# Kernel optimization log

Measured on AMD Instinct MI355X. Metric: run time of the kernel, lower is better.

## Reference

```python
import jax, jax.numpy as jnp
import numpy as np

N = 50000
NUM_GRAPHS = 64
EPS = 1e-16  # PyG softmax denominator epsilon


def _gat_conv(x, src, dst, W, a_src, a_dst, b, heads, out_ch):
    n = x.shape[0]
    h = (x @ W).reshape(n, heads, out_ch)                    # [N,H,C]
    al_s = jnp.einsum('nhc,hc->nh', h, a_src)                # [N,H]
    al_d = jnp.einsum('nhc,hc->nh', h, a_dst)                # [N,H]
    e = jax.nn.leaky_relu(al_s[src] + al_d[dst], 0.2)        # [E,H]
    emax = jax.ops.segment_max(e, dst, num_segments=n)       # [N,H]
    ee = jnp.exp(e - emax[dst])
    den = jax.ops.segment_sum(ee, dst, num_segments=n)       # [N,H]
    alpha = ee / (den[dst] + EPS)                            # [E,H]
    msg = h[src] * alpha[:, :, None]                         # [E,H,C]
    out = jax.ops.segment_sum(msg, dst, num_segments=n)      # [N,H,C]
    return out.reshape(n, heads * out_ch) + b


def setup_inputs() -> dict:
    key = jax.random.key(0)
    ks = jax.random.split(key, 16)
    E = 250000
    x = jax.random.normal(ks[0], (N, 11), dtype=jnp.float32)
    edge_index = jax.random.randint(ks[1], (2, E), 0, N, dtype=jnp.int64)
    batch = jnp.sort(jax.random.randint(ks[2], (N,), 0, NUM_GRAPHS, dtype=jnp.int64))
    def glorot(k, shape):
        fan = shape[0] + shape[-1]
        return jax.random.uniform(k, shape, jnp.float32, -1.0, 1.0) * np.sqrt(6.0 / fan)
    return {
        'x': x, 'edge_index': edge_index, 'batch': batch,
        'W1': glorot(ks[3], (11, 8 * 128)),
        'a1s': glorot(ks[4], (8, 128)), 'a1d': glorot(ks[5], (8, 128)),
        'b1': jnp.zeros((8 * 128,), jnp.float32),
        'W2': glorot(ks[6], (1024, 8 * 64)),
        'a2s': glorot(ks[7], (8, 64)), 'a2d': glorot(ks[8], (8, 64)),
        'b2': jnp.zeros((8 * 64,), jnp.float32),
        'W3': glorot(ks[9], (512, 4 * 32)),
        'a3s': glorot(ks[10], (4, 32)), 'a3d': glorot(ks[11], (4, 32)),
        'b3': jnp.zeros((4 * 32,), jnp.float32),
        'Wout': glorot(ks[12], (128, 1)),
        'bout': jnp.zeros((1,), jnp.float32),
    }


def reference(x, edge_index, batch, W1, a1s, a1d, b1, W2, a2s, a2d, b2,
              W3, a3s, a3d, b3, Wout, bout):
    n = x.shape[0]
    # GATConv adds self-loops by default
    loop = jnp.arange(n, dtype=edge_index.dtype)
    src = jnp.concatenate([edge_index[0], loop])
    dst = jnp.concatenate([edge_index[1], loop])
    h = jax.nn.leaky_relu(_gat_conv(x, src, dst, W1, a1s, a1d, b1, 8, 128), 0.01)
    h = jax.nn.leaky_relu(_gat_conv(h, src, dst, W2, a2s, a2d, b2, 8, 64), 0.01)
    h = jax.nn.leaky_relu(_gat_conv(h, src, dst, W3, a3s, a3d, b3, 4, 32), 0.01)
    # global mean pool over graphs
    sums = jax.ops.segment_sum(h, batch, num_segments=NUM_GRAPHS)      # [G,128]
    cnt = jax.ops.segment_sum(jnp.ones((n,), h.dtype), batch, num_segments=NUM_GRAPHS)
    pooled = sums / jnp.maximum(cnt, 1.0)[:, None]
    return pooled @ Wout + bout                                        # [G,1]
```

## Files before the change

### kernel.cpp

```cpp
#include <hip/hip_runtime.h>

#define EPS 1e-16f

typedef __attribute__((ext_vector_type(8))) short short8;
typedef __attribute__((ext_vector_type(4))) float f32x4;

__device__ __forceinline__ float b2f(unsigned short u) {
    return __uint_as_float(((unsigned)u) << 16);
}
__device__ __forceinline__ unsigned short f2b(float f) {
    unsigned u = __float_as_uint(f);
    u += 0x7fffu + ((u >> 16) & 1u);
    return (unsigned short)(u >> 16);
}

typedef __attribute__((address_space(3))) void lds_vp;
typedef __attribute__((address_space(1))) const void glb_vp;
__device__ __forceinline__ void load_lds16(const unsigned short* g,
                                           unsigned short* l) {
    __builtin_amdgcn_global_load_lds((glb_vp*)g, (lds_vp*)l, 16, 0, 0);
}

__global__ void setup_kernel(const float* __restrict__ W1,
                             const float* __restrict__ W2,
                             const float* __restrict__ W3,
                             unsigned short* __restrict__ wt2,
                             unsigned short* __restrict__ wt3,
                             unsigned short* __restrict__ w1sk,
                             const float* __restrict__ a1s,
                             const float* __restrict__ a1d,
                             float* __restrict__ w_as,
                             float* __restrict__ w_ad, int* __restrict__ deg,
                             float* __restrict__ pool, int N, int GC, int WB,
                             int DB, int PB) {
    int b = blockIdx.x, t = threadIdx.x;
    if (b < WB) {
        int i = b * 256 + t;
        if (i < 1024 * 512) {
            int k = i / 512, n = i % 512;
            wt2[(size_t)n * 1024 + k] = f2b(W2[i]);
        } else if (i < 1024 * 512 + 512 * 128) {
            int j = i - 1024 * 512;
            int k = j / 128, n = j % 128;
            wt3[(size_t)n * 512 + k] = f2b(W3[j]);
        } else if (i < 1024 * 512 + 512 * 128 + 8 * 128 * 32) {
            int q = i - (1024 * 512 + 512 * 128);
            int h = q >> 12, rem = q & 4095;
            int c = rem >> 5, kk = rem & 31;
            int off = (h == 7) ? 16 : 0;
            float v = 0.f;
            int k = kk - off;
            if (k >= 0 && k < 11) v = W1[k * 1024 + h * 128 + c];
            w1sk[q] = f2b(v);
        }
    } else if (b < WB + DB) {
        int i = (b - WB) * 256 + t;
        if (i < N) deg[i] = 1;
    } else if (b < WB + DB + PB) {
        int i = (b - WB - DB) * 256 + t;
        if (i < GC) pool[i] = 0.f;
    } else {
        if (t < 88) {
            int h = t / 11, k = t % 11;
            float s = 0.f, d = 0.f;
            for (int c = 0; c < 128; c++) {
                float w = W1[k * 1024 + h * 128 + c];
                s += w * a1s[h * 128 + c];
                d += w * a1d[h * 128 + c];
            }
            w_as[h * 16 + k] = s;
            w_ad[h * 16 + k] = d;
        }
    }
}

__global__ void hist_al1_kernel(const int* __restrict__ ei, int E, int N,
                                int* __restrict__ deg,
                                const float* __restrict__ x,
                                const float* __restrict__ w_as,
                                const float* __restrict__ w_ad,
                                float* __restrict__ als,
                                float* __restrict__ ald, int EB) {
    int b = blockIdx.x, t = threadIdx.x;
    if (b < EB) {
        int e = b * 256 + t;
        if (e < E) {
            int d = ei[E + e];
            if ((unsigned)d < (unsigned)N) atomicAdd(&deg[d], 1);
        }
    } else {
        int i = (b - EB) * 256 + t;
        if (i < N * 8) {
            int n = i >> 3, h = i & 7;
            float s = 0.f, d = 0.f;
#pragma unroll
            for (int k = 0; k < 11; k++) {
                float xv = x[n * 11 + k];
                s += xv * w_as[h * 16 + k];
                d += xv * w_ad[h * 16 + k];
            }
            als[i] = s;
            ald[i] = d;
        }
    }
}

__global__ void scan_block_kernel(const int* __restrict__ deg,
                                  int* __restrict__ rowst,
                                  int* __restrict__ bsum, int N) {
    __shared__ int s[256];
    int t = threadIdx.x, b = blockIdx.x;
    int i = b * 256 + t;
    s[t] = (i < N) ? deg[i] : 0;
    __syncthreads();
    for (int o = 1; o < 256; o <<= 1) {
        int a = (t >= o) ? s[t - o] : 0;
        __syncthreads();
        s[t] += a;
        __syncthreads();
    }
    if (i < N) rowst[i + 1] = s[t];
    if (t == 255) bsum[b] = s[255];
}

__global__ void scan_top_kernel(const int* __restrict__ bsum,
                                int* __restrict__ boff, int NB) {
    __shared__ int psum[65];
    int t = threadIdx.x;
    int chunk = (NB + 63) / 64;
    int lo = t * chunk, hi = lo + chunk;
    if (lo > NB) lo = NB;
    if (hi > NB) hi = NB;
    int s = 0;
    for (int i = lo; i < hi; i++) s += bsum[i];
    psum[t + 1] = s;
    __syncthreads();
    if (t == 0) {
        psum[0] = 0;
        for (int i = 1; i <= 64; i++) psum[i] += psum[i - 1];
    }
    __syncthreads();
    int run = psum[t];
    for (int i = lo; i < hi; i++) {
        boff[i] = run;
        run += bsum[i];
    }
}

__global__ void scan_finish_kernel(int* __restrict__ rowst,
                                   const int* __restrict__ boff,
                                   const int* __restrict__ deg,
                                   int* __restrict__ srcs,
                                   int* __restrict__ cursor, int N) {
    int i = blockIdx.x * 256 + threadIdx.x;
    if (i == 0) rowst[0] = 0;
    if (i < N) {
        int incl = rowst[i + 1] + boff[blockIdx.x];
        rowst[i + 1] = incl;
        int st = incl - deg[i];
        srcs[st] = i;
        cursor[i] = st + 1;
    }
}

__global__ void scatter_kernel(const int* __restrict__ ei, int E, int N,
                               int* cursor, int* srcs) {
    int e = blockIdx.x * blockDim.x + threadIdx.x;
    if (e < E) {
        int d = ei[E + e];
        if ((unsigned)d < (unsigned)N) {
            int p = atomicAdd(&cursor[d], 1);
            int s = ei[e];
            if ((unsigned)s >= (unsigned)N) s = d;
            srcs[p] = s;
        }
    }
}

__global__ void agg1_fused(const float* __restrict__ x,
                           const float* __restrict__ als,
                           const float* __restrict__ ald,
                           const int* __restrict__ rowst,
                           const int* __restrict__ srcs,
                           unsigned short* __restrict__ A2, int N) {
    constexpr int MAXE = 64;
    __shared__ float sv[MAXE * 8];
    __shared__ float sx[MAXE * 12];
    int n = blockIdx.x;
    int t = threadIdx.x;
    int h = t >> 4, k = t & 15;
    int start = rowst[n], end = rowst[n + 1];
    int deg = end - start;
    float acc = 0.f;

    if (deg <= MAXE) {
        for (int p = t; p < deg * 8; p += 128) {
            int e = p >> 3, hh = p & 7;
            int s = srcs[start + e];
            float v = als[s * 8 + hh] + ald[n * 8 + hh];
            sv[e * 8 + hh] = v > 0.f ? v : 0.2f * v;
        }
        for (int p = t; p < deg * 16; p += 128) {
            int e = p >> 4, kx = p & 15;
            if (kx < 11)
                sx[e * 12 + kx] = x[(size_t)srcs[start + e] * 11 + kx];
        }
        __syncthreads();
        float m = -1e30f;
        for (int e = k; e < deg; e += 16) m = fmaxf(m, sv[e * 8 + h]);
#pragma unroll
        for (int o = 1; o < 16; o <<= 1) m = fmaxf(m, __shfl_xor(m, o));
        float ee[(MAXE + 15) / 16];
        float den = 0.f;
        {
            int kk = 0;
            for (int e = k; e < deg; e += 16, kk++) {
                float xv = expf(sv[e * 8 + h] - m);
                ee[kk] = xv;
                den += xv;
            }
        }
#pragma unroll
        for (int o = 1; o < 16; o <<= 1) den += __shfl_xor(den, o);
        float dinv = 1.0f / (den + EPS);
        {
            int kk = 0;
            for (int e = k; e < deg; e += 16, kk++)
                sv[e * 8 + h] = ee[kk] * dinv;
        }
        __syncthreads();
        const int CH = 4;
        for (int e = 0; e < deg; e += CH) {
            int mc = deg - e;
            if (mc > CH) mc = CH;
            float al[CH], xv[CH];
#pragma unroll
            for (int j = 0; j < CH; j++)
                if (j < mc) {
                    al[j] = sv[(e + j) * 8 + h];
                    xv[j] = (k < 11) ? sx[(e + j) * 12 + k] : 0.f;
                }
#pragma unroll
            for (int j = 0; j < CH; j++)
                if (j < mc) acc += al[j] * xv[j];
        }
    } else {
        float aldn = ald[n * 8 + h];
        float m = -1e30f;
        for (int idx = start + k; idx < end; idx += 16) {
            float v = als[srcs[idx] * 8 + h] + aldn;
            v = v > 0.f ? v : 0.2f * v;
            m = fmaxf(m, v);
        }
#pragma unroll
        for (int o = 1; o < 16; o <<= 1) m = fmaxf(m, __shfl_xor(m, o));
        float den = 0.f;
        for (int idx = start + k; idx < end; idx += 16) {
            float v = als[srcs[idx] * 8 + h] + aldn;
            v = v > 0.f ? v : 0.2f * v;
            den += expf(v - m);
        }
#pragma unroll
        for (int o = 1; o < 16; o <<= 1) den += __shfl_xor(den, o);
        float dinv = 1.0f / (den + EPS);
        for (int idx = start; idx < end; idx++) {
            int s = srcs[idx];
            float v = als[s * 8 + h] + aldn;
            v = v > 0.f ? v : 0.2f * v;
            float a = expf(v - m) * dinv;
            float xv = (k < 11) ? x[s * 11 + k] : 0.f;
            acc += a * xv;
        }
    }
    A2[(size_t)n * 128 + t] = f2b(acc);
}

template <bool EPI, int HB, int CC, bool SK>
__global__ __launch_bounds__(256) void gemm_mfma(
    const unsigned short* __restrict__ A, const unsigned short* __restrict__ Bt,
    unsigned short* __restrict__ C, const float* __restrict__ bias,
    const float* __restrict__ a_s, const float* __restrict__ a_d,
    float* __restrict__ als, float* __restrict__ ald, int H, int M, int N,
    int K, int lda) {
    int NX = gridDim.x;
    int bid = blockIdx.y * NX + blockIdx.x;
    int win = bid & (8 * NX - 1);
    int mg = bid / (8 * NX);
    int m_t = mg * 8 + (win & 7);
    int n_t = win >> 3;
    int bm = m_t * 128, bn = n_t * 128;
    if (bm >= M) return;

    union SMem {
        struct {
            unsigned short As[2][128 * 32];
            unsigned short Bs[2][128 * 32];
        } k;
        unsigned short Ct[128 * 132];
    };
    __shared__ __align__(16) SMem sm;
    auto& As = sm.k.As;
    auto& Bs = sm.k.Bs;
    auto& Ct = sm.Ct;

    int t = threadIdx.x;
    int w = t >> 6, lane = t & 63;
    int quad = lane >> 4, l16 = lane & 15;
    int wr = (w >> 1) * 64, wc = (w & 1) * 64;

    int kofs = 0;
    const unsigned short* Bb = Bt;
    if (SK) {
        kofs = n_t * 16;
        if (kofs > lda - 32) kofs = lda - 32;
        Bb = Bt + (size_t)n_t * 128 * 32;
    }

    int c0 = w * 128 + lane;
    int c1 = c0 + 64;
    int r0 = c0 >> 2, p0 = c0 & 3;
    int r1 = c1 >> 2, p1 = c1 & 3;
    int j0 = (p0 - (r0 >> 1)) & 3;
    int j1 = (p1 - (r1 >> 1)) & 3;
    int ga0 = bm + r0;
    if (ga0 >= M) ga0 = M - 1;
    int ga1 = bm + r1;
    if (ga1 >= M) ga1 = M - 1;
    const unsigned short* Ag0 = A + (size_t)ga0 * lda + kofs + j0 * 8;
    const unsigned short* Ag1 = A + (size_t)ga1 * lda + kofs + j1 * 8;
    size_t br0 = SK ? (size_t)r0 : (size_t)(bn + r0);
    size_t br1 = SK ? (size_t)r1 : (size_t)(bn + r1);
    const unsigned short* Bg0 = Bb + br0 * K + j0 * 8;
    const unsigned short* Bg1 = Bb + br1 * K + j1 * 8;

    auto stage = [&](int st, int k0) {
        load_lds16(Ag0 + k0, &As[st][(w * 128) * 8]);
        load_lds16(Ag1 + k0, &As[st][(w * 128 + 64) * 8]);
        load_lds16(Bg0 + k0, &Bs[st][(w * 128) * 8]);
        load_lds16(Bg1 + k0, &Bs[st][(w * 128 + 64) * 8]);
    };

    int aoff[4], boff4[4];
#pragma unroll
    for (int i = 0; i < 4; i++) {
        int ra = wr + i * 16 + l16;
        aoff[i] = ra * 32 + (((quad + (ra >> 1)) & 3) * 8);
        int rb = wc + i * 16 + l16;
        boff4[i] = rb * 32 + (((quad + (rb >> 1)) & 3) * 8);
    }

    f32x4 acc[4][4] = {};
    stage(0, 0);
    int st = 0;
    for (int k0 = 0; k0 < K; k0 += 32, st ^= 1) {
        __syncthreads();
        if (k0 + 32 < K) stage(st ^ 1, k0 + 32);
        short8 a[4], b[4];
#pragma unroll
        for (int mi = 0; mi < 4; mi++) a[mi] = *(const short8*)&As[st][aoff[mi]];
#pragma unroll
        for (int ni = 0; ni < 4; ni++) b[ni] = *(const short8*)&Bs[st][boff4[ni]];
#pragma unroll
        for (int mi = 0; mi < 4; mi++)
#pragma unroll
            for (int ni = 0; ni < 4; ni++)
                acc[mi][ni] = __builtin_amdgcn_mfma_f32_16x16x32_bf16(
                    a[mi], b[ni], acc[mi][ni], 0, 0, 0);
    }
    __syncthreads();

#pragma unroll
    for (int mi = 0; mi < 4; mi++) {
#pragma unroll
        for (int r = 0; r < 4; r++) {
            int rl = wr + mi * 16 + quad * 4 + r;
#pragma unroll
            for (int ni = 0; ni < 4; ni++) {
                int cl = wc + ni * 16 + l16;
                float v = acc[mi][ni][r];
                if (EPI) {
                    v += bias[bn + cl];
                    v = v > 0.f ? v : 0.01f * v;
                }
                Ct[rl * 132 + cl] = f2b(v);
            }
        }
    }
    __syncthreads();
#pragma unroll
    for (int p = 0; p < 16; p++) {
        int q = p * 256 + t;
        int row = q >> 5, c8 = q & 31;
        if (bm + row < M) {
            uint2 v = *(const uint2*)&Ct[row * 132 + c8 * 4];
            *(uint2*)&C[(size_t)(bm + row) * N + bn + c8 * 4] = v;
        }
    }
    if (HB > 0) {
        for (int pi = t; pi < 128 * HB; pi += 256) {
            int row = pi / HB, hl = pi % HB;
            if (bm + row >= M) continue;
            int hg = bn / CC + hl;
            const unsigned short* rp = &Ct[row * 132 + hl * CC];
            const float* asp = a_s + hg * CC;
            const float* adp = a_d + hg * CC;
            float s = 0.f, d = 0.f;
#pragma unroll
            for (int c = 0; c < CC; c++) {
                float v = b2f(rp[c]);
                s += v * asp[c];
                d += v * adp[c];
            }
            als[(size_t)(bm + row) * H + hg] = s;
            ald[(size_t)(bm + row) * H + hg] = d;
        }
    }
}

template <int HB, int CC>
__global__ __launch_bounds__(256, 2) void gemm_pipe(
    const unsigned short* __restrict__ A, const unsigned short* __restrict__ Bt,
    unsigned short* __restrict__ C, const float* __restrict__ a_s,
    const float* __restrict__ a_d, float* __restrict__ als,
    float* __restrict__ ald, int H, int M, int N, int K) {
    int NX = gridDim.x;
    int bid = blockIdx.y * NX + blockIdx.x;
    int win = bid & (8 * NX - 1);
    int mg = bid / (8 * NX);
    int m_t = mg * 8 + (win & 7);
    int n_t = win >> 3;
    int bm = m_t * 128, bn = n_t * 128;
    if (bm >= M) return;

    union SMem {
        struct {
            unsigned short As[2][128 * 64];
            unsigned short Bs[2][128 * 64];
        } k;
        unsigned short Ct[128 * 132];
    };
    __shared__ __align__(16) SMem sm;

    int t = threadIdx.x;
    int w = t >> 6, lane = t & 63;
    int quad = lane >> 4, l16 = lane & 15;
    int wr = (w >> 1) * 64, wc = (w & 1) * 64;

    int srow = lane >> 3;
    int gsl = (lane & 7) ^ srow;
    const unsigned short* Ag[4];
    const unsigned short* Bg[4];
#pragma unroll
    for (int j = 0; j < 4; j++) {
        int row = (j * 4 + w) * 8 + srow;
        int ga = bm + row;
        if (ga > M - 1) ga = M - 1;
        Ag[j] = A + (size_t)ga * K + gsl * 8;
        Bg[j] = Bt + (size_t)(bn + row) * K + gsl * 8;
    }
    auto stage = [&](int st, int kt) {
        int ko = kt * 64;
#pragma unroll
        for (int j = 0; j < 4; j++) {
            load_lds16(Ag[j] + ko, &sm.k.As[st][(j * 4 + w) * 512]);
            load_lds16(Bg[j] + ko, &sm.k.Bs[st][(j * 4 + w) * 512]);
        }
    };

    int arow[4], brow[4];
#pragma unroll
    for (int i = 0; i < 4; i++) {
        arow[i] = (wr + i * 16 + l16) * 64;
        brow[i] = (wc + i * 16 + l16) * 64;
    }
    int sw = l16 & 7;

    f32x4 acc[4][4] = {};
    int NT = K >> 6;
    stage(0, 0);
    if (NT > 1) stage(1, 1);
    for (int tt = 0; tt < NT; tt++) {
        int bb = tt & 1;
        if (tt + 1 < NT)
            asm volatile("s_waitcnt vmcnt(8)" ::: "memory");
        else
            asm volatile("s_waitcnt vmcnt(0)" ::: "memory");
        __builtin_amdgcn_s_barrier();
        __builtin_amdgcn_sched_barrier(0);
#pragma unroll
        for (int ks = 0; ks < 2; ks++) {
            short8 a[4], b[4];
            int so = ((ks * 4 + quad) ^ sw) * 8;
#pragma unroll
            for (int mi = 0; mi < 4; mi++)
                a[mi] = *(const short8*)&sm.k.As[bb][arow[mi] + so];
#pragma unroll
            for (int ni = 0; ni < 4; ni++)
                b[ni] = *(const short8*)&sm.k.Bs[bb][brow[ni] + so];
            __builtin_amdgcn_s_setprio(1);
#pragma unroll
            for (int mi = 0; mi < 4; mi++)
#pragma unroll
                for (int ni = 0; ni < 4; ni++)
                    acc[mi][ni] = __builtin_amdgcn_mfma_f32_16x16x32_bf16(
                        a[mi], b[ni], acc[mi][ni], 0, 0, 0);
            __builtin_amdgcn_s_setprio(0);
        }
        asm volatile("s_waitcnt lgkmcnt(0)" ::: "memory");
        __builtin_amdgcn_s_barrier();
        if (tt + 2 < NT) stage(bb, tt + 2);
    }
    __syncthreads();

#pragma unroll
    for (int mi = 0; mi < 4; mi++) {
#pragma unroll
        for (int r = 0; r < 4; r++) {
            int rl = wr + mi * 16 + quad * 4 + r;
#pragma unroll
            for (int ni = 0; ni < 4; ni++) {
                int cl = wc + ni * 16 + l16;
                sm.Ct[rl * 132 + cl] = f2b(acc[mi][ni][r]);
            }
        }
    }
    __syncthreads();
#pragma unroll
    for (int p = 0; p < 16; p++) {
        int q = p * 256 + t;
        int row = q >> 5, c8 = q & 31;
        if (bm + row < M) {
            uint2 v = *(const uint2*)&sm.Ct[row * 132 + c8 * 4];
            *(uint2*)&C[(size_t)(bm + row) * N + bn + c8 * 4] = v;
        }
    }
    if (HB > 0) {
        for (int pi = t; pi < 128 * HB; pi += 256) {
            int row = pi / HB, hl = pi % HB;
            if (bm + row >= M) continue;
            int hg = bn / CC + hl;
            const unsigned short* rp = &sm.Ct[row * 132 + hl * CC];
            const float* asp = a_s + hg * CC;
            const float* adp = a_d + hg * CC;
            float s = 0.f, d = 0.f;
#pragma unroll
            for (int c = 0; c < CC; c++) {
                float v = b2f(rp[c]);
                s += v * asp[c];
                d += v * adp[c];
            }
            als[(size_t)(bm + row) * H + hg] = s;
            ald[(size_t)(bm + row) * H + hg] = d;
        }
    }
}

template <int H, int C>
__global__ void agg_fused4(const unsigned short* __restrict__ hin,
                           const float* __restrict__ als,
                           const float* __restrict__ ald,
                           const int* __restrict__ rowst,
                           const int* __restrict__ srcs,
                           const float* __restrict__ bias,
                           unsigned short* __restrict__ out, int N) {
    constexpr int HC = H * C;
    constexpr int NT = HC / 4;
    constexpr int TPH = C / 4;
    constexpr int MAXE = 64;
    __shared__ float sv[MAXE * H];
    __shared__ int ssrc[MAXE];
    int n = blockIdx.x;
    int t = threadIdx.x;
    int c = t * 4;
    int hh = c / C;
    int li = (c % C) / 4;
    int start = rowst[n], end = rowst[n + 1];
    int deg = end - start;
    float a0 = 0.f, a1 = 0.f, a2 = 0.f, a3 = 0.f;

    if (deg <= MAXE) {
        for (int p = t; p < deg * H; p += NT) {
            int e = p / H, h = p % H;
            int s = srcs[start + e];
            if (h == 0) ssrc[e] = s;
            float v = als[s * H + h] + ald[n * H + h];
            sv[e * H + h] = v > 0.f ? v : 0.2f * v;
        }
        __syncthreads();
        float m = -1e30f;
        for (int e = li; e < deg; e += TPH) m = fmaxf(m, sv[e * H + hh]);
#pragma unroll
        for (int o = 1; o < TPH; o <<= 1) m = fmaxf(m, __shfl_xor(m, o));
        float ee[(MAXE + TPH - 1) / TPH];
        float den = 0.f;
        {
            int k = 0;
            for (int e = li; e < deg; e += TPH, k++) {
                float x = expf(sv[e * H + hh] - m);
                ee[k] = x;
                den += x;
            }
        }
#pragma unroll
        for (int o = 1; o < TPH; o <<= 1) den += __shfl_xor(den, o);
        float dinv = 1.0f / (den + EPS);
        {
            int k = 0;
            for (int e = li; e < deg; e += TPH, k++)
                sv[e * H + hh] = ee[k] * dinv;
        }
        __syncthreads();
        const int CH = 4;
        for (int e = 0; e < deg; e += CH) {
            int mc = deg - e;
            if (mc > CH) mc = CH;
            int ss[CH];
            float al[CH];
            ushort4 uv[CH];
#pragma unroll
            for (int j = 0; j < CH; j++)
                if (j < mc) {
                    ss[j] = ssrc[e + j];
                    al[j] = sv[(e + j) * H + hh];
                }
#pragma unroll
            for (int j = 0; j < CH; j++)
                if (j < mc)
                    uv[j] = *(const ushort4*)(hin + (size_t)ss[j] * HC + c);
#pragma unroll
            for (int j = 0; j < CH; j++)
                if (j < mc) {
                    a0 += al[j] * b2f(uv[j].x);
                    a1 += al[j] * b2f(uv[j].y);
                    a2 += al[j] * b2f(uv[j].z);
                    a3 += al[j] * b2f(uv[j].w);
                }
        }
    } else {
        float aldn = ald[n * H + hh];
        float m = -1e30f;
        for (int idx = start + li; idx < end; idx += TPH) {
            float v = als[srcs[idx] * H + hh] + aldn;
            v = v > 0.f ? v : 0.2f * v;
            m = fmaxf(m, v);
        }
#pragma unroll
        for (int o = 1; o < TPH; o <<= 1) m = fmaxf(m, __shfl_xor(m, o));
        float den = 0.f;
        for (int idx = start + li; idx < end; idx += TPH) {
            float v = als[srcs[idx] * H + hh] + aldn;
            v = v > 0.f ? v : 0.2f * v;
            den += expf(v - m);
        }
#pragma unroll
        for (int o = 1; o < TPH; o <<= 1) den += __shfl_xor(den, o);
        float dinv = 1.0f / (den + EPS);
        const int CH = 4;
        for (int idx = start; idx < end; idx += CH) {
            int mc = end - idx;
            if (mc > CH) mc = CH;
            int ss[CH];
            float lv[CH];
            ushort4 uv[CH];
#pragma unroll
            for (int j = 0; j < CH; j++)
                if (j < mc) ss[j] = srcs[idx + j];
#pragma unroll
            for (int j = 0; j < CH; j++)
                if (j < mc) lv[j] = als[ss[j] * H + hh];
#pragma unroll
            for (int j = 0; j < CH; j++)
                if (j < mc)
                    uv[j] = *(const ushort4*)(hin + (size_t)ss[j] * HC + c);
#pragma unroll
            for (int j = 0; j < CH; j++)
                if (j < mc) {
                    float v = lv[j] + aldn;
                    v = v > 0.f ? v : 0.2f * v;
                    float a = expf(v - m) * dinv;
                    a0 += a * b2f(uv[j].x);
                    a1 += a * b2f(uv[j].y);
                    a2 += a * b2f(uv[j].z);
                    a3 += a * b2f(uv[j].w);
                }
        }
    }
    float v0 = a0 + bias[c], v1 = a1 + bias[c + 1];
    float v2 = a2 + bias[c + 2], v3 = a3 + bias[c + 3];
    ushort4 o;
    o.x = f2b(v0 > 0.f ? v0 : 0.01f * v0);
    o.y = f2b(v1 > 0.f ? v1 : 0.01f * v1);
    o.z = f2b(v2 > 0.f ? v2 : 0.01f * v2);
    o.w = f2b(v3 > 0.f ? v3 : 0.01f * v3);
    *(ushort4*)&out[(size_t)n * HC + c] = o;
}

template <int H, int C>
__global__ void agg_fused2(const unsigned short* __restrict__ hin,
                           const float* __restrict__ als,
                           const float* __restrict__ ald,
                           const int* __restrict__ rowst,
                           const int* __restrict__ srcs,
                           const float* __restrict__ bias,
                           unsigned short* __restrict__ out, int N) {
    constexpr int HC = H * C;
    constexpr int NT = HC / 2;
    constexpr int TPH = C / 2;
    constexpr int MAXE = 64;
    __shared__ float sv[MAXE * H];
    __shared__ int ssrc[MAXE];
    int n = blockIdx.x;
    int t = threadIdx.x;
    int c = t * 2;
    int hh = c / C;
    int li = (c % C) / 2;
    int start = rowst[n], end = rowst[n + 1];
    int deg = end - start;
    float a0 = 0.f, a1 = 0.f;

    if (deg <= MAXE) {
        for (int p = t; p < deg * H; p += NT) {
            int e = p / H, h = p % H;
            int s = srcs[start + e];
            if (h == 0) ssrc[e] = s;
            float v = als[s * H + h] + ald[n * H + h];
            sv[e * H + h] = v > 0.f ? v : 0.2f * v;
        }
        __syncthreads();
        float m = -1e30f;
        for (int e = li; e < deg; e += TPH) m = fmaxf(m, sv[e * H + hh]);
#pragma unroll
        for (int o = 1; o < TPH; o <<= 1) m = fmaxf(m, __shfl_xor(m, o));
        float ee[(MAXE + TPH - 1) / TPH];
        float den = 0.f;
        {
            int k = 0;
            for (int e = li; e < deg; e += TPH, k++) {
                float x = expf(sv[e * H + hh] - m);
                ee[k] = x;
                den += x;
            }
        }
#pragma unroll
        for (int o = 1; o < TPH; o <<= 1) den += __shfl_xor(den, o);
        float dinv = 1.0f / (den + EPS);
        {
            int k = 0;
            for (int e = li; e < deg; e += TPH, k++)
                sv[e * H + hh] = ee[k] * dinv;
        }
        __syncthreads();
        const int CH = 4;
        for (int e = 0; e < deg; e += CH) {
            int mc = deg - e;
            if (mc > CH) mc = CH;
            int ss[CH];
            float al[CH];
            ushort2 uv[CH];
#pragma unroll
            for (int j = 0; j < CH; j++)
                if (j < mc) {
                    ss[j] = ssrc[e + j];
                    al[j] = sv[(e + j) * H + hh];
                }
#pragma unroll
            for (int j = 0; j < CH; j++)
                if (j < mc)
                    uv[j] = *(const ushort2*)(hin + (size_t)ss[j] * HC + c);
#pragma unroll
            for (int j = 0; j < CH; j++)
                if (j < mc) {
                    a0 += al[j] * b2f(uv[j].x);
                    a1 += al[j] * b2f(uv[j].y);
                }
        }
    } else {
        float aldn = ald[n * H + hh];
        float m = -1e30f;
        for (int idx = start + li; idx < end; idx += TPH) {
            float v = als[srcs[idx] * H + hh] + aldn;
            v = v > 0.f ? v : 0.2f * v;
            m = fmaxf(m, v);
        }
#pragma unroll
        for (int o = 1; o < TPH; o <<= 1) m = fmaxf(m, __shfl_xor(m, o));
        float den = 0.f;
        for (int idx = start + li; idx < end; idx += TPH) {
            float v = als[srcs[idx] * H + hh] + aldn;
            v = v > 0.f ? v : 0.2f * v;
            den += expf(v - m);
        }
#pragma unroll
        for (int o = 1; o < TPH; o <<= 1) den += __shfl_xor(den, o);
        float dinv = 1.0f / (den + EPS);
        const int CH = 4;
        for (int idx = start; idx < end; idx += CH) {
            int mc = end - idx;
            if (mc > CH) mc = CH;
            int ss[CH];
            float lv[CH];
            ushort2 uv[CH];
#pragma unroll
            for (int j = 0; j < CH; j++)
                if (j < mc) ss[j] = srcs[idx + j];
#pragma unroll
            for (int j = 0; j < CH; j++)
                if (j < mc) lv[j] = als[ss[j] * H + hh];
#pragma unroll
            for (int j = 0; j < CH; j++)
                if (j < mc)
                    uv[j] = *(const ushort2*)(hin + (size_t)ss[j] * HC + c);
#pragma unroll
            for (int j = 0; j < CH; j++)
                if (j < mc) {
                    float v = lv[j] + aldn;
                    v = v > 0.f ? v : 0.2f * v;
                    float a = expf(v - m) * dinv;
                    a0 += a * b2f(uv[j].x);
                    a1 += a * b2f(uv[j].y);
                }
        }
    }
    float v0 = a0 + bias[c], v1 = a1 + bias[c + 1];
    ushort2 o;
    o.x = f2b(v0 > 0.f ? v0 : 0.01f * v0);
    o.y = f2b(v1 > 0.f ? v1 : 0.01f * v1);
    *(ushort2*)&out[(size_t)n * HC + c] = o;
}

__global__ void pool_partial_kernel(const unsigned short* __restrict__ h3,
                                    const int* __restrict__ batch,
                                    float* __restrict__ pool, int N, int G) {
    int lo = blockIdx.x * 128;
    int hi = lo + 128;
    if (hi > N) hi = N;
    if (lo >= N) return;
    int t = threadIdx.x;
    int cur = batch[lo];
    float acc = 0.f;
    for (int n = lo; n < hi; n++) {
        int g = batch[n];
        if (g != cur) {
            if ((unsigned)cur < (unsigned)G) atomicAdd(&pool[cur * 128 + t], acc);
            acc = 0.f;
            cur = g;
        }
        acc += b2f(h3[(size_t)n * 128 + t]);
    }
    if ((unsigned)cur < (unsigned)G) atomicAdd(&pool[cur * 128 + t], acc);
}

__global__ void head_kernel(const float* __restrict__ pool,
                            const int* __restrict__ batch,
                            const float* __restrict__ Wout,
                            const float* __restrict__ bout,
                            float* __restrict__ out, int N) {
    int g = blockIdx.x;
    int t = threadIdx.x;
    int lo, hi;
    {
        int a = 0, b = N;
        while (a < b) { int mid = (a + b) >> 1; if (batch[mid] < g) a = mid + 1; else b = mid; }
        lo = a;
        a = lo; b = N;
        while (a < b) { int mid = (a + b) >> 1; if (batch[mid] < g + 1) a = mid + 1; else b = mid; }
        hi = a;
    }
    float c = (float)(hi - lo);
    c = c > 1.f ? c : 1.f;
    float v = (pool[g * 128 + t] / c) * Wout[t];
    for (int o = 32; o; o >>= 1) v += __shfl_xor(v, o);
    __shared__ float partial[2];
    if ((t & 63) == 0) partial[t >> 6] = v;
    __syncthreads();
    if (t == 0) out[g] = partial[0] + partial[1] + bout[0];
}

extern "C" void kernel_launch(void* const* d_in, const int* in_sizes, int n_in,
                              void* d_out, int out_size, void* d_ws,
                              size_t ws_size, hipStream_t stream) {
    const float* x = (const float*)d_in[0];
    const int* ei = (const int*)d_in[1];
    const int* batch = (const int*)d_in[2];
    const float* W1 = (const float*)d_in[3];
    const float* a1s = (const float*)d_in[4];
    const float* a1d = (const float*)d_in[5];
    const float* b1 = (const float*)d_in[6];
    const float* W2 = (const float*)d_in[7];
    const float* a2s = (const float*)d_in[8];
    const float* a2d = (const float*)d_in[9];
    const float* b2 = (const float*)d_in[10];
    const float* W3 = (const float*)d_in[11];
    const float* a3s = (const float*)d_in[12];
    const float* a3d = (const float*)d_in[13];
    const float* b3 = (const float*)d_in[14];
    const float* Wout = (const float*)d_in[15];
    const float* bout = (const float*)d_in[16];
    float* out = (float*)d_out;

    const int N = in_sizes[0] / 11;
    const int E = in_sizes[1] / 2;
    const int Etot = E + N;
    const int G = out_size;
    const int NB = (N + 255) / 256;
    const int MT = ((N + 127) / 128 + 7) / 8 * 8;

    char* ws = (char*)d_ws;
    size_t off = 0;
    auto alloc = [&](size_t bytes) -> void* {
        void* p = ws + off;
        off += (bytes + 255) & ~(size_t)255;
        return p;
    };
    unsigned short* buf1 = (unsigned short*)alloc((size_t)N * 1024 * 2);
    unsigned short* buf2 = (unsigned short*)alloc((size_t)N * 1024 * 2);
    float* als = (float*)alloc((size_t)N * 8 * 4);
    float* ald = (float*)alloc((size_t)N * 8 * 4);
    int* rowst = (int*)alloc((size_t)(N + 1) * 4);
    int* cursor = (int*)alloc((size_t)N * 4);
    int* srcs = (int*)alloc((size_t)Etot * 4);
    int* deg = (int*)alloc((size_t)N * 4);
    int* bsum = (int*)alloc((size_t)NB * 4);
    int* boff = (int*)alloc((size_t)NB * 4);
    float* pool = (float*)alloc((size_t)G * 128 * 4);
    unsigned short* aggx = (unsigned short*)alloc((size_t)N * 128 * 2);
    unsigned short* w1sk = (unsigned short*)alloc((size_t)8 * 128 * 32 * 2);
    unsigned short* wt2 = (unsigned short*)alloc((size_t)1024 * 512 * 2);
    unsigned short* wt3 = (unsigned short*)alloc((size_t)512 * 128 * 2);
    float* w_as = (float*)alloc(8 * 16 * 4);
    float* w_ad = (float*)alloc(8 * 16 * 4);

    int nb = (N + 255) / 256;
    int eb = (E + 255) / 256;

    const int WTOT = 1024 * 512 + 512 * 128 + 8 * 128 * 32;
    const int WB = (WTOT + 255) / 256;
    const int PB = (G * 128 + 255) / 256;
    setup_kernel<<<WB + nb + PB + 1, 256, 0, stream>>>(
        W1, W2, W3, wt2, wt3, w1sk, a1s, a1d, w_as, w_ad, deg, pool, N,
        G * 128, WB, nb, PB);

    const int AB = (N * 8 + 255) / 256;
    hist_al1_kernel<<<eb + AB, 256, 0, stream>>>(ei, E, N, deg, x, w_as, w_ad,
                                                 als, ald, eb);

    scan_block_kernel<<<NB, 256, 0, stream>>>(deg, rowst, bsum, N);
    scan_top_kernel<<<1, 64, 0, stream>>>(bsum, boff, NB);
    scan_finish_kernel<<<NB, 256, 0, stream>>>(rowst, boff, deg, srcs, cursor,
                                               N);
    scatter_kernel<<<eb, 256, 0, stream>>>(ei, E, N, cursor, srcs);

    agg1_fused<<<N, 128, 0, stream>>>(x, als, ald, rowst, srcs, aggx, N);
    gemm_mfma<true, 0, 1, true><<<dim3(8, MT), 256, 0, stream>>>(
        aggx, w1sk, buf2, b1, nullptr, nullptr, nullptr, nullptr, 0, N, 1024,
        32, 128);

    gemm_pipe<2, 64><<<dim3(4, MT), 256, 0, stream>>>(
        buf2, wt2, buf1, a2s, a2d, als, ald, 8, N, 512, 1024);
    agg_fused4<8, 64><<<N, 128, 0, stream>>>(buf1, als, ald, rowst, srcs, b2,
                                             buf2, N);

    gemm_pipe<4, 32><<<dim3(1, MT), 256, 0, stream>>>(
        buf2, wt3, buf1, a3s, a3d, als, ald, 4, N, 128, 512);
    agg_fused2<4, 32><<<N, 64, 0, stream>>>(buf1, als, ald, rowst, srcs, b3,
                                            buf2, N);

    pool_partial_kernel<<<(N + 127) / 128, 128, 0, stream>>>(buf2, batch, pool,
                                                             N, G);
    head_kernel<<<G, 128, 0, stream>>>(pool, batch, Wout, bout, out, N);
}
```

Baseline: 432.8 us.

## Fuse CSR build into cooperative kernel and widen layer-2 aggregation to 8 channels

Replaces the separate histogram, three scan kernels and scatter kernel with a single cooperative-launch kernel that uses grid-wide syncs between phases, cutting several launches and inter-kernel gaps. Separately, the layer-2 aggregation kernel now processes 8 bf16 channels per thread with 16-byte loads and launches 64 threads per node instead of 128. The per-node fallback loop for large degrees is simplified to one edge at a time. Cooperative launch with one block per 256 edges may exceed the co-residency limit and fail to launch, and halving threads per node lowers parallelism per block.

```diff
diff --git a/kernel.cpp b/kernel.cpp
--- a/kernel.cpp
+++ b/kernel.cpp
@@ -1,4 +1,7 @@
 #include <hip/hip_runtime.h>
+#include <hip/hip_cooperative_groups.h>
+
+namespace cg = cooperative_groups;
 
 #define EPS 1e-16f
 
@@ -30,9 +33,9 @@
                              const float* __restrict__ a1s,
                              const float* __restrict__ a1d,
                              float* __restrict__ w_as,
-                             float* __restrict__ w_ad, int* __restrict__ deg,
-                             float* __restrict__ pool, int N, int GC, int WB,
-                             int DB, int PB) {
+                             float* __restrict__ w_ad,
+                             float* __restrict__ pool, int GC, int WB,
+                             int PB) {
     int b = blockIdx.x, t = threadIdx.x;
     if (b < WB) {
         int i = b * 256 + t;
@@ -53,11 +56,8 @@
             if (k >= 0 && k < 11) v = W1[k * 1024 + h * 128 + c];
             w1sk[q] = f2b(v);
         }
-    } else if (b < WB + DB) {
+    } else if (b < WB + PB) {
         int i = (b - WB) * 256 + t;
-        if (i < N) deg[i] = 1;
-    } else if (b < WB + DB + PB) {
-        int i = (b - WB - DB) * 256 + t;
         if (i < GC) pool[i] = 0.f;
     } else {
         if (t < 88) {
@@ -74,105 +74,107 @@
     }
 }
 
-__global__ void hist_al1_kernel(const int* __restrict__ ei, int E, int N,
-                                int* __restrict__ deg,
-                                const float* __restrict__ x,
-                                const float* __restrict__ w_as,
-                                const float* __restrict__ w_ad,
-                                float* __restrict__ als,
-                                float* __restrict__ ald, int EB) {
-    int b = blockIdx.x, t = threadIdx.x;
-    if (b < EB) {
-        int e = b * 256 + t;
-        if (e < E) {
-            int d = ei[E + e];
-            if ((unsigned)d < (unsigned)N) atomicAdd(&deg[d], 1);
-        }
-    } else {
-        int i = (b - EB) * 256 + t;
-        if (i < N * 8) {
-            int n = i >> 3, h = i & 7;
-            float s = 0.f, d = 0.f;
-#pragma unroll
-            for (int k = 0; k < 11; k++) {
-                float xv = x[n * 11 + k];
-                s += xv * w_as[h * 16 + k];
-                d += xv * w_ad[h * 16 + k];
+__global__ void csr_coop(const int* __restrict__ ei, int E, int N,
+                         int* __restrict__ deg, int* __restrict__ rowst,
+                         int* __restrict__ bsum, int* __restrict__ boff,
+                         int* __restrict__ srcs, int* __restrict__ cursor,
+                         const float* __restrict__ x,
+                         const float* __restrict__ w_as,
+                         const float* __restrict__ w_ad,
+                         float* __restrict__ als, float* __restrict__ ald,
+                         int NB) {
+    cg::grid_group grid = cg::this_grid();
+    int nbk = gridDim.x;
+    int t = threadIdx.x;
+    int gtid = blockIdx.x * 256 + t;
+    int gstride = nbk * 256;
+    __shared__ int s[256];
+    __shared__ int psum[65];
+
+    for (int i = gtid; i < N; i += gstride) deg[i] = 1;
+    grid.sync();
+
+    for (int e = gtid; e < E; e += gstride) {
+        int d = ei[E + e];
+        if ((unsigned)d < (unsigned)N) atomicAdd(&deg[d], 1);
+    }
+    for (int i = gtid; i < N * 8; i += gstride) {
+        int n = i >> 3, h = i & 7;
+        float sa = 0.f, da = 0.f;
+#pragma unroll
+        for (int k = 0; k < 11; k++) {
+            float xv = x[n * 11 + k];
+            sa += xv * w_as[h * 16 + k];
+            da += xv * w_ad[h * 16 + k];
+        }
+        als[i] = sa;
+        ald[i] = da;
+    }
+    grid.sync();
+
+    for (int b = blockIdx.x; b < NB; b += nbk) {
+        int i = b * 256 + t;
+        s[t] = (i < N) ? deg[i] : 0;
+        __syncthreads();
+        for (int o = 1; o < 256; o <<= 1) {
+            int a = (t >= o) ? s[t - o] : 0;
+            __syncthreads();
+            s[t] += a;
+            __syncthreads();
+        }
+        if (i < N) rowst[i + 1] = s[t];
+        if (t == 255) bsum[b] = s[255];
+        __syncthreads();
+    }
+    grid.sync();
+
+    if (blockIdx.x == 0) {
+        int chunk = (NB + 63) / 64;
+        int lo = 0, hi = 0, acc = 0;
+        if (t < 64) {
+            lo = t * chunk;
+            hi = lo + chunk;
+            if (lo > NB) lo = NB;
+            if (hi > NB) hi = NB;
+            for (int i = lo; i < hi; i++) acc += bsum[i];
+            psum[t + 1] = acc;
+        }
+        __syncthreads();
+        if (t == 0) {
+            psum[0] = 0;
+            for (int i = 1; i <= 64; i++) psum[i] += psum[i - 1];
+        }
+        __syncthreads();
+        if (t < 64) {
+            int run = psum[t];
+            for (int i = lo; i < hi; i++) {
+                boff[i] = run;
+                run += bsum[i];
             }
-            als[i] = s;
-            ald[i] = d;
-        }
-    }
-}
-
-__global__ void scan_block_kernel(const int* __restrict__ deg,
-                                  int* __restrict__ rowst,
-                                  int* __restrict__ bsum, int N) {
-    __shared__ int s[256];
-    int t = threadIdx.x, b = blockIdx.x;
-    int i = b * 256 + t;
-    s[t] = (i < N) ? deg[i] : 0;
-    __syncthreads();
-    for (int o = 1; o < 256; o <<= 1) {
-        int a = (t >= o) ? s[t - o] : 0;
-        __syncthreads();
-        s[t] += a;
-        __syncthreads();
-    }
-    if (i < N) rowst[i + 1] = s[t];
-    if (t == 255) bsum[b] = s[255];
-}
-
-__global__ void scan_top_kernel(const int* __restrict__ bsum,
-                                int* __restrict__ boff, int NB) {
-    __shared__ int psum[65];
-    int t = threadIdx.x;
-    int chunk = (NB + 63) / 64;
-    int lo = t * chunk, hi = lo + chunk;
-    if (lo > NB) lo = NB;
-    if (hi > NB) hi = NB;
-    int s = 0;
-    for (int i = lo; i < hi; i++) s += bsum[i];
-    psum[t + 1] = s;
-    __syncthreads();
-    if (t == 0) {
-        psum[0] = 0;
-        for (int i = 1; i <= 64; i++) psum[i] += psum[i - 1];
-    }
-    __syncthreads();
-    int run = psum[t];
-    for (int i = lo; i < hi; i++) {
-        boff[i] = run;
-        run += bsum[i];
-    }
-}
-
-__global__ void scan_finish_kernel(int* __restrict__ rowst,
-                                   const int* __restrict__ boff,
-                                   const int* __restrict__ deg,
-                                   int* __restrict__ srcs,
-                                   int* __restrict__ cursor, int N) {
-    int i = blockIdx.x * 256 + threadIdx.x;
-    if (i == 0) rowst[0] = 0;
-    if (i < N) {
-        int incl = rowst[i + 1] + boff[blockIdx.x];
-        rowst[i + 1] = incl;
-        int st = incl - deg[i];
-        srcs[st] = i;
-        cursor[i] = st + 1;
-    }
-}
-
-__global__ void scatter_kernel(const int* __restrict__ ei, int E, int N,
-                               int* cursor, int* srcs) {
-    int e = blockIdx.x * blockDim.x + threadIdx.x;
-    if (e < E) {
+        }
+    }
+    grid.sync();
+
+    for (int b = blockIdx.x; b < NB; b += nbk) {
+        int i = b * 256 + t;
+        if (i == 0) rowst[0] = 0;
+        if (i < N) {
+            int incl = rowst[i + 1] + boff[b];
+            rowst[i + 1] = incl;
+            int st = incl - deg[i];
+            srcs[st] = i;
+            cursor[i] = st + 1;
+        }
+    }
+    grid.sync();
+
+    for (int e = gtid; e < E; e += gstride) {
         int d = ei[E + e];
         if ((unsigned)d < (unsigned)N) {
             int p = atomicAdd(&cursor[d], 1);
-            int s = ei[e];
-            if ((unsigned)s >= (unsigned)N) s = d;
-            srcs[p] = s;
+            int sv = ei[e];
+            if ((unsigned)sv >= (unsigned)N) sv = d;
+            srcs[p] = sv;
         }
     }
 }
@@ -564,19 +566,19 @@
                            const float* __restrict__ bias,
                            unsigned short* __restrict__ out, int N) {
     constexpr int HC = H * C;
-    constexpr int NT = HC / 4;
-    constexpr int TPH = C / 4;
+    constexpr int NT = HC / 8;
+    constexpr int TPH = C / 8;
     constexpr int MAXE = 64;
     __shared__ float sv[MAXE * H];
     __shared__ int ssrc[MAXE];
     int n = blockIdx.x;
     int t = threadIdx.x;
-    int c = t * 4;
+    int c = t * 8;
     int hh = c / C;
-    int li = (c % C) / 4;
+    int li = (c % C) / 8;
     int start = rowst[n], end = rowst[n + 1];
     int deg = end - start;
-    float a0 = 0.f, a1 = 0.f, a2 = 0.f, a3 = 0.f;
+    float acc[8] = {};
 
     if (deg <= MAXE) {
         for (int p = t; p < deg * H; p += NT) {
@@ -616,7 +618,7 @@
             if (mc > CH) mc = CH;
             int ss[CH];
             float al[CH];
-            ushort4 uv[CH];
+            short8 uv[CH];
 #pragma unroll
             for (int j = 0; j < CH; j++)
                 if (j < mc) {
@@ -626,14 +628,14 @@
 #pragma unroll
             for (int j = 0; j < CH; j++)
                 if (j < mc)
-                    uv[j] = *(const ushort4*)(hin + (size_t)ss[j] * HC + c);
+                    uv[j] = *(const short8*)(hin + (size_t)ss[j] * HC + c);
 #pragma unroll
             for (int j = 0; j < CH; j++)
                 if (j < mc) {
-                    a0 += al[j] * b2f(uv[j].x);
-                    a1 += al[j] * b2f(uv[j].y);
-                    a2 += al[j] * b2f(uv[j].z);
-                    a3 += al[j] * b2f(uv[j].w);
+                    float a = al[j];
+#pragma unroll
+                    for (int q = 0; q < 8; q++)
+                        acc[q] += a * b2f((unsigned short)uv[j][q]);
                 }
         }
     } else {
@@ -655,44 +657,25 @@
 #pragma unroll
         for (int o = 1; o < TPH; o <<= 1) den += __shfl_xor(den, o);
         float dinv = 1.0f / (den + EPS);
-        const int CH = 4;
-        for (int idx = start; idx < end; idx += CH) {
-            int mc = end - idx;
-            if (mc > CH) mc = CH;
-            int ss[CH];
-            float lv[CH];
-            ushort4 uv[CH];
-#pragma unroll
-            for (int j = 0; j < CH; j++)
-                if (j < mc) ss[j] = srcs[idx + j];
-#pragma unroll
-            for (int j = 0; j < CH; j++)
-                if (j < mc) lv[j] = als[ss[j] * H + hh];
-#pragma unroll
-            for (int j = 0; j < CH; j++)
-                if (j < mc)
-                    uv[j] = *(const ushort4*)(hin + (size_t)ss[j] * HC + c);
-#pragma unroll
-            for (int j = 0; j < CH; j++)
-                if (j < mc) {
-                    float v = lv[j] + aldn;
-                    v = v > 0.f ? v : 0.2f * v;
-                    float a = expf(v - m) * dinv;
-                    a0 += a * b2f(uv[j].x);
-                    a1 += a * b2f(uv[j].y);
-                    a2 += a * b2f(uv[j].z);
-                    a3 += a * b2f(uv[j].w);
-                }
-        }
-    }
-    float v0 = a0 + bias[c], v1 = a1 + bias[c + 1];
-    float v2 = a2 + bias[c + 2], v3 = a3 + bias[c + 3];
-    ushort4 o;
-    o.x = f2b(v0 > 0.f ? v0 : 0.01f * v0);
-    o.y = f2b(v1 > 0.f ? v1 : 0.01f * v1);
-    o.z = f2b(v2 > 0.f ? v2 : 0.01f * v2);
-    o.w = f2b(v3 > 0.f ? v3 : 0.01f * v3);
-    *(ushort4*)&out[(size_t)n * HC + c] = o;
+        for (int idx = start; idx < end; idx++) {
+            int s = srcs[idx];
+            float v = als[s * H + hh] + aldn;
+            v = v > 0.f ? v : 0.2f * v;
+            float a = expf(v - m) * dinv;
+            short8 uv = *(const short8*)(hin + (size_t)s * HC + c);
+#pragma unroll
+            for (int q = 0; q < 8; q++)
+                acc[q] += a * b2f((unsigned short)uv[q]);
+        }
+    }
+    short8 o8;
+#pragma unroll
+    for (int q = 0; q < 8; q++) {
+        float v = acc[q] + bias[c + q];
+        v = v > 0.f ? v : 0.01f * v;
+        o8[q] = (short)f2b(v);
+    }
+    *(short8*)&out[(size_t)n * HC + c] = o8;
 }
 
 template <int H, int C>
@@ -930,25 +913,26 @@
     float* w_as = (float*)alloc(8 * 16 * 4);
     float* w_ad = (float*)alloc(8 * 16 * 4);
 
-    int nb = (N + 255) / 256;
     int eb = (E + 255) / 256;
 
     const int WTOT = 1024 * 512 + 512 * 128 + 8 * 128 * 32;
     const int WB = (WTOT + 255) / 256;
     const int PB = (G * 128 + 255) / 256;
-    setup_kernel<<<WB + nb + PB + 1, 256, 0, stream>>>(
-        W1, W2, W3, wt2, wt3, w1sk, a1s, a1d, w_as, w_ad, deg, pool, N,
-        G * 128, WB, nb, PB);
-
-    const int AB = (N * 8 + 255) / 256;
-    hist_al1_kernel<<<eb + AB, 256, 0, stream>>>(ei, E, N, deg, x, w_as, w_ad,
-                                                 als, ald, eb);
-
-    scan_block_kernel<<<NB, 256, 0, stream>>>(deg, rowst, bsum, N);
-    scan_top_kernel<<<1, 64, 0, stream>>>(bsum, boff, NB);
-    scan_finish_kernel<<<NB, 256, 0, stream>>>(rowst, boff, deg, srcs, cursor,
-                                               N);
-    scatter_kernel<<<eb, 256, 0, stream>>>(ei, E, N, cursor, srcs);
+    setup_kernel<<<WB + PB + 1, 256, 0, stream>>>(W1, W2, W3, wt2, wt3, w1sk,
+                                                  a1s, a1d, w_as, w_ad, pool,
+                                                  G * 128, WB, PB);
+
+    {
+        int GB = eb;
+        int Ev = E, Nv = N, NBv = NB;
+        void* args[] = {(void*)&ei,   (void*)&Ev,     (void*)&Nv,
+                        (void*)&deg,  (void*)&rowst,  (void*)&bsum,
+                        (void*)&boff, (void*)&srcs,   (void*)&cursor,
+                        (void*)&x,    (void*)&w_as,   (void*)&w_ad,
+                        (void*)&als,  (void*)&ald,    (void*)&NBv};
+        hipLaunchCooperativeKernel((void*)csr_coop, dim3(GB), dim3(256), args,
+                                   0, stream);
+    }
 
     agg1_fused<<<N, 128, 0, stream>>>(x, als, ald, rowst, srcs, aggx, N);
     gemm_mfma<true, 0, 1, true><<<dim3(8, MT), 256, 0, stream>>>(
@@ -957,8 +941,8 @@
 
     gemm_pipe<2, 64><<<dim3(4, MT), 256, 0, stream>>>(
         buf2, wt2, buf1, a2s, a2d, als, ald, 8, N, 512, 1024);
-    agg_fused4<8, 64><<<N, 128, 0, stream>>>(buf1, als, ald, rowst, srcs, b2,
-                                             buf2, N);
+    agg_fused4<8, 64><<<N, 64, 0, stream>>>(buf1, als, ald, rowst, srcs, b2,
+                                            buf2, N);
 
     gemm_pipe<4, 32><<<dim3(1, MT), 256, 0, stream>>>(
         buf2, wt3, buf1, a3s, a3d, als, ald, 4, N, 128, 512);
```

Result: slower. 910.4 us (+110.3%).
